# Kernel tuning notes

Measured on AMD Instinct MI355X. Metric: run time of the kernel, lower is better.

Reference implementation:

```python
import jax, jax.numpy as jnp
import numpy as np

NUM_HEADS = 16
HEAD_DIM = 64
LN_EPS = 1e-12


def _interleave_pairs(a, b):
    # stack([a, b], -1).reshape(..., 2*d) -> interleaved on last dim
    return jnp.stack([a, b], axis=-1).reshape(a.shape[:-1] + (a.shape[-1] * 2,))


def _rotate_half(x):
    # stack([-x[..., 1::2], x[..., ::2]], -1).reshape_as(x)
    return _interleave_pairs(-x[..., 1::2], x[..., ::2])


def setup_inputs() -> dict:
    key = jax.random.key(0)
    ks = jax.random.split(key, 4)
    B, S, H = 4, 2048, 1024
    hidden_states = jax.random.normal(ks[0], (B, S, H), dtype=jnp.float32)
    sinusoidal_pos = jax.random.uniform(ks[1], (1, 1, S, HEAD_DIM), dtype=jnp.float32)
    ln_weight = jnp.ones((H,), dtype=jnp.float32)
    ln_bias = jnp.zeros((H,), dtype=jnp.float32)
    w_qkv = jax.random.normal(ks[2], (H, 3 * H), dtype=jnp.float32) * (1.0 / np.sqrt(H))
    b_qkv = jax.random.normal(ks[3], (3 * H,), dtype=jnp.float32) * 0.02
    return {"hidden_states": hidden_states, "sinusoidal_pos": sinusoidal_pos,
            "ln_weight": ln_weight, "ln_bias": ln_bias, "w_qkv": w_qkv, "b_qkv": b_qkv}


def reference(hidden_states, sinusoidal_pos, ln_weight, ln_bias, w_qkv, b_qkv):
    B, S, H = hidden_states.shape
    # LayerNorm
    mu = jnp.mean(hidden_states, axis=-1, keepdims=True)
    var = jnp.mean(jnp.square(hidden_states - mu), axis=-1, keepdims=True)
    h = (hidden_states - mu) * jax.lax.rsqrt(var + LN_EPS) * ln_weight + ln_bias
    # Fused QKV projection
    qkv = h @ w_qkv + b_qkv                       # [B, S, 3H]
    q, k, v = jnp.split(qkv, 3, axis=-1)
    def to_heads(x):
        return x.reshape(B, S, NUM_HEADS, HEAD_DIM).transpose(0, 2, 1, 3)  # [B, Hn, S, D]
    q, k, v = to_heads(q), to_heads(k), to_heads(v)
    # RoPE (RoFormer interleaved style)
    sin, cos = jnp.split(sinusoidal_pos, 2, axis=-1)      # each [1,1,S,D/2]
    sin_pos = _interleave_pairs(sin, sin)                 # [1,1,S,D]
    cos_pos = _interleave_pairs(cos, cos)
    q = q * cos_pos + _rotate_half(q) * sin_pos
    k = k * cos_pos + _rotate_half(k) * sin_pos
    # SDPA (non-causal, no mask, eval-mode dropout=0)
    scale = 1.0 / np.sqrt(HEAD_DIM)
    scores = jnp.einsum('bhqd,bhkd->bhqk', q, k) * scale
    probs = jax.nn.softmax(scores, axis=-1)
    ctx = jnp.einsum('bhqk,bhkd->bhqd', probs, v)         # [B, Hn, S, D]
    ctx = ctx.transpose(0, 2, 1, 3).reshape(B, S, H)
    return ctx
```

## Files before the change

### kernel.cpp

```cpp
#include <hip/hip_runtime.h>
#include <hip/hip_bf16.h>
#include <cstdint>
#include <cstddef>

#define DEVINL __device__ __forceinline__

typedef float f32x2 __attribute__((ext_vector_type(2)));
typedef float f32x4 __attribute__((ext_vector_type(4)));
typedef float f32x16 __attribute__((ext_vector_type(16)));
typedef short s16x8 __attribute__((ext_vector_type(8)));
typedef short s16x4 __attribute__((ext_vector_type(4)));

static constexpr int Sd = 2048;
static constexpr int Hd = 1024;
static constexpr int NHd = 16;
static constexpr int Dd = 64;
static constexpr int N3 = 3072;

DEVINL float bf2f(short u){
  unsigned int t = ((unsigned int)(unsigned short)u) << 16;
  float f; __builtin_memcpy(&f, &t, 4); return f;
}
DEVINL short f2bf(float f){
  unsigned int t; __builtin_memcpy(&t, &f, 4);
  unsigned int r = t + 0x7FFFu + ((t >> 16) & 1u);
  return (short)(r >> 16);
}

DEVINL void gld16(const short* g, short* l){
  __builtin_amdgcn_global_load_lds((const __attribute__((address_space(1))) unsigned int*)g,
                                   (__attribute__((address_space(3))) unsigned int*)l, 16, 0, 0);
}

DEVINL int cvtpk(float lo, float hi){
  int r; asm("v_cvt_pk_bf16_f32 %0, %1, %2" : "=v"(r) : "v"(lo), "v"(hi)); return r;
}

DEVINL float fexp2(float x){
#if __has_builtin(__builtin_amdgcn_exp2f)
  return __builtin_amdgcn_exp2f(x);
#else
  return exp2f(x);
#endif
}

DEVINL f32x16 z16(){
  f32x16 v;
  #pragma unroll
  for (int i=0;i<16;i++) v[i]=0.f;
  return v;
}

__global__ __launch_bounds__(256) void ln_kernel(const float* __restrict__ x,
                                                 const float* __restrict__ w,
                                                 const float* __restrict__ bs,
                                                 short* __restrict__ h){
  int row = blockIdx.x, tid = threadIdx.x;
  const float* xr = x + (size_t)row * Hd;
  f32x4 v = *(const f32x4*)(xr + tid*4);
  float s1 = v[0]+v[1]+v[2]+v[3];
  float s2 = v[0]*v[0]+v[1]*v[1]+v[2]*v[2]+v[3]*v[3];
  #pragma unroll
  for (int off = 1; off < 64; off <<= 1){ s1 += __shfl_xor(s1, off); s2 += __shfl_xor(s2, off); }
  __shared__ float red[8];
  if ((tid & 63) == 0){ red[(tid>>6)*2] = s1; red[(tid>>6)*2+1] = s2; }
  __syncthreads();
  s1 = red[0]+red[2]+red[4]+red[6];
  s2 = red[1]+red[3]+red[5]+red[7];
  float mu = s1 * (1.0f/Hd);
  float rstd = rsqrtf(s2*(1.0f/Hd) - mu*mu + 1e-12f);
  f32x4 wv = *(const f32x4*)(w + tid*4);
  f32x4 bv = *(const f32x4*)(bs + tid*4);
  s16x4 o;
  #pragma unroll
  for (int i=0;i<4;i++) o[i] = f2bf((v[i]-mu)*rstd*wv[i] + bv[i]);
  *(s16x4*)(h + (size_t)row*Hd + tid*4) = o;
}

__global__ __launch_bounds__(256) void castw_kernel(const float* __restrict__ w, short* __restrict__ wT){
  __shared__ float t[32][33];
  int n0 = blockIdx.x*32, k0 = blockIdx.y*32;
  int tx = threadIdx.x, ty = threadIdx.y;
  #pragma unroll
  for (int i=0;i<4;i++) t[ty + i*8][tx] = w[(size_t)(k0 + ty + i*8)*N3 + n0 + tx];
  __syncthreads();
  #pragma unroll
  for (int i=0;i<4;i++) wT[(size_t)(n0 + ty + i*8)*Hd + k0 + tx] = f2bf(t[tx][ty + i*8]);
}

__global__ __launch_bounds__(256) void gemm_kernel(const short* __restrict__ A,
                                                   const short* __restrict__ Bt,
                                                   const float* __restrict__ bias,
                                                   const float* __restrict__ sp,
                                                   short* __restrict__ qo,
                                                   short* __restrict__ ko,
                                                   short* __restrict__ vo){
  __shared__ alignas(16) char smem[33792];
  short* lA = (short*)smem;
  short* lB = (short*)(smem + 8192);
  float* sps2 = (float*)smem;
  int bid = blockIdx.x;
  int xcd = bid & 7, idx = bid >> 3;
  int mt = xcd*8 + (idx & 7), nt = idx >> 3;
  int m0 = mt*128, n0 = nt*128;
  int tid = threadIdx.x, lane = tid & 63, wv = tid >> 6;
  int l15 = lane & 15, lq = lane >> 4;
  int wr = wv >> 1, wc = wv & 1;
  f32x4 zero = {0.f,0.f,0.f,0.f};
  f32x4 acc[4][4];
  #pragma unroll
  for (int m=0;m<4;m++)
    #pragma unroll
    for (int n=0;n<4;n++) acc[m][n] = zero;
  int flat = tid*8;
  int row0 = flat >> 5, col0 = flat & 31;
  const short* ga = A  + (size_t)(m0 + row0)*Hd + col0;
  const short* gb = Bt + (size_t)(n0 + row0)*Hd + col0;
  short* lAw = lA + wv*512;
  short* lBw = lB + wv*512;
  for (int kk = 0; kk < Hd; kk += 32){
    __syncthreads();
    gld16(ga + kk,                 lAw);
    gld16(ga + kk + (size_t)64*Hd, lAw + 2048);
    gld16(gb + kk,                 lBw);
    gld16(gb + kk + (size_t)64*Hd, lBw + 2048);
    __syncthreads();
    s16x8 af[4], bf[4];
    #pragma unroll
    for (int m=0;m<4;m++) af[m] = *(const s16x8*)(lA + (wr*64 + m*16 + l15)*32 + 8*lq);
    #pragma unroll
    for (int n=0;n<4;n++) bf[n] = *(const s16x8*)(lB + (wc*64 + n*16 + l15)*32 + 8*lq);
    #pragma unroll
    for (int m=0;m<4;m++)
      #pragma unroll
      for (int n=0;n<4;n++)
        acc[m][n] = __builtin_amdgcn_mfma_f32_16x16x32_bf16(af[m], bf[n], acc[m][n], 0, 0, 0);
  }
  int part = nt >> 3;
  if (part == 2){
    #pragma unroll
    for (int n=0;n<4;n++){
      int c = n0 + wc*64 + n*16 + l15;
      float bv = bias[c];
      int hh = (c >> 6) & 15, d = c & 63;
      #pragma unroll
      for (int m=0;m<4;m++){
        int r0 = m0 + wr*64 + m*16 + lq*4;
        int b = r0 >> 11, s0r = r0 & 2047;
        s16x4 o;
        #pragma unroll
        for (int j=0;j<4;j++) o[j] = f2bf(acc[m][n][j] + bv);
        *(s16x4*)(vo + (((size_t)((b*NHd + hh)*Dd + d)) << 11) + s0r) = o;
      }
    }
  } else {
    __syncthreads();
    const float* gsp = sp + (size_t)(m0 & 2047)*64;
    #pragma unroll
    for (int u4=0; u4<4; ++u4){
      int u = tid + u4*256;
      int sl = u >> 3, dh4 = u & 7;
      f32x4 s4v = *(const f32x4*)(gsp + sl*64 + dh4*4);
      f32x4 c4v = *(const f32x4*)(gsp + sl*64 + 32 + dh4*4);
      float* w8 = sps2 + sl*66 + dh4*8;
      f32x2 p0 = {s4v[0], c4v[0]}, p1 = {s4v[1], c4v[1]};
      f32x2 p2 = {s4v[2], c4v[2]}, p3 = {s4v[3], c4v[3]};
      *(f32x2*)(w8)     = p0; *(f32x2*)(w8 + 2) = p1;
      *(f32x2*)(w8 + 4) = p2; *(f32x2*)(w8 + 6) = p3;
    }
    __syncthreads();
    short* dst = part == 0 ? qo : ko;
    float postscale = part == 0 ? 0.18033688011112042f : 1.0f;
    float sgnmul = (l15 & 1) ? 1.0f : -1.0f;
    float bvv[4]; int hhv[4], dv[4];
    #pragma unroll
    for (int n=0;n<4;n++){
      int c = n0 + wc*64 + n*16 + l15;
      bvv[n] = bias[c]; hhv[n] = (c >> 6) & 15; dv[n] = c & 63;
    }
    int dh0 = l15 >> 1;
    #pragma unroll
    for (int m=0;m<4;m++){
      #pragma unroll
      for (int j=0;j<4;j++){
        int sl = wr*64 + m*16 + lq*4 + j;
        const float* sb = sps2 + sl*66 + dh0*2;
        int r = m0 + sl;
        int b = r >> 11, s = r & 2047;
        #pragma unroll
        for (int n=0;n<4;n++){
          f32x2 sc = *(const f32x2*)(sb + n*16);
          float x = acc[m][n][j] + bvv[n];
          float xp = __shfl_xor(x, 1);
          float y = (x*sc[1] + sgnmul*xp*sc[0]) * postscale;
          dst[(((size_t)((b*NHd + hhv[n])*Sd + s)) << 6) + dv[n]] = f2bf(y);
        }
      }
    }
  }
}

__global__ __launch_bounds__(512, 4) void attn_kernel(const short* __restrict__ q,
                                                      const short* __restrict__ k,
                                                      const short* __restrict__ vT,
                                                      float* __restrict__ out){
  __shared__ alignas(16) short kbuf[2][8192];
  __shared__ alignas(16) short vbuf[2][8192];
  int bid = blockIdx.x;
  int xcd = bid & 7, w = bid >> 3;
  int bh = xcd*8 + (w >> 3), qb = w & 7;
  int tid = threadIdx.x, lane = tid & 63, wv = tid >> 6;
  int l31 = lane & 31, hi = lane >> 5;
  const short* kp = k  + ((size_t)bh << 17);
  const short* vp = vT + ((size_t)bh << 17);
  int qrow = qb*256 + wv*32 + l31;
  const short* qp = q + ((size_t)bh << 17) + (size_t)qrow*64;
  s16x8 qf[4];
  #pragma unroll
  for (int kk=0;kk<4;kk++) qf[kk] = *(const s16x8*)(qp + kk*16 + hi*8);
  int kc0 = tid,      kr0 = kc0 >> 3;
  int kc1 = tid+512,  kr1 = kc1 >> 3;
  int koff0 = kr0*64 + ((kc0 ^ kr0) & 7)*8;
  int koff1 = kr1*64 + ((kc1 ^ kr1) & 7)*8;
  int vr0 = tid >> 4,       vcc0 = tid & 15;
  int vr1 = (tid+512) >> 4, vcc1 = (tid+512) & 15;
  int voff0 = vr0*2048 + ((vcc0 & 8) | ((vcc0 ^ vr0) & 7))*8;
  int voff1 = vr1*2048 + ((vcc1 & 8) | ((vcc1 ^ vr1) & 7))*8;

  f32x16 ot0 = z16(), ot1 = z16();
  float m = -1e30f, lr = 0.f;
  int rsw = (l31 & 7);

#define STAGE(nb, t) do { \
    gld16(kp + (size_t)(t)*8192 + koff0, &kbuf[nb][0]    + wv*512); \
    gld16(kp + (size_t)(t)*8192 + koff1, &kbuf[nb][4096] + wv*512); \
    gld16(vp + (size_t)(t)*128  + voff0, &vbuf[nb][0]    + wv*512); \
    gld16(vp + (size_t)(t)*128  + voff1, &vbuf[nb][4096] + wv*512); \
  } while(0)

  STAGE(0, 0);
  __syncthreads();

  for (int t = 0; t < 16; ++t){
    int cur = t & 1;
    if (t < 15) STAGE(cur^1, t+1);
    #pragma unroll
    for (int h = 0; h < 2; ++h){
      const short* kb = &kbuf[cur][h*4096];
      const short* vb = &vbuf[cur][h*64];
      f32x16 s0 = z16(), s1 = z16();
      __builtin_amdgcn_s_setprio(1);
      #pragma unroll
      for (int kk=0;kk<4;kk++){
        s16x8 kf0 = *(const s16x8*)(kb + l31*64       + (((kk*2 + hi) ^ rsw)*8));
        s0 = __builtin_amdgcn_mfma_f32_32x32x16_bf16(kf0, qf[kk], s0, 0, 0, 0);
        s16x8 kf1 = *(const s16x8*)(kb + (32+l31)*64  + (((kk*2 + hi) ^ rsw)*8));
        s1 = __builtin_amdgcn_mfma_f32_32x32x16_bf16(kf1, qf[kk], s1, 0, 0, 0);
      }
      __builtin_amdgcn_s_setprio(0);
      float tm[16];
      #pragma unroll
      for (int i=0;i<16;i++) tm[i] = fmaxf(s0[i], s1[i]);
      #pragma unroll
      for (int off=8; off>=1; off>>=1)
        #pragma unroll
        for (int i=0;i<off;i++) tm[i] = fmaxf(tm[i], tm[i+off]);
      float pmax = fmaxf(tm[0], __shfl_xor(tm[0], 32));
      if (!__all(pmax - m <= 8.0f)){
        float mn = fmaxf(m, pmax);
        float al = fexp2(m - mn);
        m = mn; lr *= al;
        #pragma unroll
        for (int i=0;i<16;i++){ ot0[i] *= al; ot1[i] *= al; }
      }
      #pragma unroll
      for (int i=0;i<16;i++){ s0[i] = fexp2(s0[i]-m); s1[i] = fexp2(s1[i]-m); }
      float ra[16];
      #pragma unroll
      for (int i=0;i<16;i++) ra[i] = s0[i] + s1[i];
      #pragma unroll
      for (int off=8; off>=1; off>>=1)
        #pragma unroll
        for (int i=0;i<off;i++) ra[i] += ra[i+off];
      lr += ra[0] + __shfl_xor(ra[0], 32);
      #pragma unroll
      for (int s4=0;s4<4;s4++){
        int base = (s4 & 1) * 8;
        int pkA0, pkA1, pkB0, pkB1;
        if (s4 < 2){
          pkA0 = cvtpk(s0[base],   s0[base+1]); pkA1 = cvtpk(s0[base+2], s0[base+3]);
          pkB0 = cvtpk(s0[base+4], s0[base+5]); pkB1 = cvtpk(s0[base+6], s0[base+7]);
        } else {
          pkA0 = cvtpk(s1[base],   s1[base+1]); pkA1 = cvtpk(s1[base+2], s1[base+3]);
          pkB0 = cvtpk(s1[base+4], s1[base+5]); pkB1 = cvtpk(s1[base+6], s1[base+7]);
        }
        int r0 = __shfl_xor(hi ? pkA0 : pkB0, 32);
        int r1 = __shfl_xor(hi ? pkA1 : pkB1, 32);
        union { int wq[4]; s16x8 v8; } u;
        u.wq[0] = hi ? r0   : pkA0;
        u.wq[1] = hi ? r1   : pkA1;
        u.wq[2] = hi ? pkB0 : r0;
        u.wq[3] = hi ? pkB1 : r1;
        __builtin_amdgcn_s_setprio(1);
        s16x8 vf0 = *(const s16x8*)(vb + l31*128      + (((s4*2 + hi) ^ rsw)*8));
        ot0 = __builtin_amdgcn_mfma_f32_32x32x16_bf16(vf0, u.v8, ot0, 0, 0, 0);
        s16x8 vf1 = *(const s16x8*)(vb + (32+l31)*128 + (((s4*2 + hi) ^ rsw)*8));
        ot1 = __builtin_amdgcn_mfma_f32_32x32x16_bf16(vf1, u.v8, ot1, 0, 0, 0);
        __builtin_amdgcn_s_setprio(0);
      }
    }
    __syncthreads();
  }
#undef STAGE
  float inv = 1.0f / lr;
  int b = bh >> 4, hh = bh & 15;
  float* orow = out + ((size_t)(b*Sd + qrow) << 10) + hh*64;
  #pragma unroll
  for (int g=0; g<4; ++g){
    f32x4 w0, w1;
    #pragma unroll
    for (int j=0;j<4;j++){ w0[j] = ot0[4*g+j]*inv; w1[j] = ot1[4*g+j]*inv; }
    *(f32x4*)(orow + g*8 + 4*hi)      = w0;
    *(f32x4*)(orow + 32 + g*8 + 4*hi) = w1;
  }
}

extern "C" void kernel_launch(void* const* d_in, const int* in_sizes, int n_in,
                              void* d_out, int out_size, void* d_ws, size_t ws_size,
                              hipStream_t stream){
  const float* hs = (const float*)d_in[0];
  const float* sp = (const float*)d_in[1];
  const float* lw = (const float*)d_in[2];
  const float* lb = (const float*)d_in[3];
  const float* wq = (const float*)d_in[4];
  const float* bq = (const float*)d_in[5];
  float* out = (float*)d_out;
  char* ws = (char*)d_ws;
  short* h   = (short*)(ws);
  short* wT  = (short*)(ws + 16777216);
  short* qb_ = (short*)(ws + 23068672);
  short* kb_ = (short*)(ws + 23068672 + 16777216);
  short* vTb = (short*)(ws + 23068672 + 33554432);

  hipLaunchKernelGGL(ln_kernel,    dim3(8192),    dim3(256),   0, stream, hs, lw, lb, h);
  hipLaunchKernelGGL(castw_kernel, dim3(96,32),   dim3(32,8),  0, stream, wq, wT);
  hipLaunchKernelGGL(gemm_kernel,  dim3(1536),    dim3(256),   0, stream, h, wT, bq, sp, qb_, kb_, vTb);
  hipLaunchKernelGGL(attn_kernel,  dim3(512),     dim3(512),   0, stream, qb_, kb_, vTb, out);
}
```

Baseline: 186.3 us.

## Process two 32-row query subtiles per wave in attention to reuse K/V fragments

```diff
diff --git a/kernel.cpp b/kernel.cpp
--- a/kernel.cpp
+++ b/kernel.cpp
@@ -200,7 +200,7 @@
   }
 }
 
-__global__ __launch_bounds__(512, 4) void attn_kernel(const short* __restrict__ q,
+__global__ __launch_bounds__(256, 2) void attn_kernel(const short* __restrict__ q,
                                                       const short* __restrict__ k,
                                                       const short* __restrict__ vT,
                                                       float* __restrict__ out){
@@ -213,29 +213,35 @@
   int l31 = lane & 31, hi = lane >> 5;
   const short* kp = k  + ((size_t)bh << 17);
   const short* vp = vT + ((size_t)bh << 17);
-  int qrow = qb*256 + wv*32 + l31;
-  const short* qp = q + ((size_t)bh << 17) + (size_t)qrow*64;
-  s16x8 qf[4];
-  #pragma unroll
-  for (int kk=0;kk<4;kk++) qf[kk] = *(const s16x8*)(qp + kk*16 + hi*8);
-  int kc0 = tid,      kr0 = kc0 >> 3;
-  int kc1 = tid+512,  kr1 = kc1 >> 3;
-  int koff0 = kr0*64 + ((kc0 ^ kr0) & 7)*8;
-  int koff1 = kr1*64 + ((kc1 ^ kr1) & 7)*8;
-  int vr0 = tid >> 4,       vcc0 = tid & 15;
-  int vr1 = (tid+512) >> 4, vcc1 = (tid+512) & 15;
-  int voff0 = vr0*2048 + ((vcc0 & 8) | ((vcc0 ^ vr0) & 7))*8;
-  int voff1 = vr1*2048 + ((vcc1 & 8) | ((vcc1 ^ vr1) & 7))*8;
-
-  f32x16 ot0 = z16(), ot1 = z16();
-  float m = -1e30f, lr = 0.f;
+  int qrowA = qb*256 + wv*64 + l31;
+  const short* qpA = q + ((size_t)bh << 17) + (size_t)qrowA*64;
+  s16x8 qf[2][4];
+  #pragma unroll
+  for (int kk=0;kk<4;kk++){
+    qf[0][kk] = *(const s16x8*)(qpA + kk*16 + hi*8);
+    qf[1][kk] = *(const s16x8*)(qpA + 2048 + kk*16 + hi*8);
+  }
+  int koff[4], voff[4];
+  #pragma unroll
+  for (int p=0;p<4;p++){
+    int c = p*256 + tid;
+    koff[p] = (c >> 3)*64 + ((c ^ (c >> 3)) & 7)*8;
+    int vr = c >> 4, vc = c & 15;
+    voff[p] = vr*2048 + ((vc & 8) | ((vc ^ vr) & 7))*8;
+  }
+
+  f32x16 ot0[2], ot1[2];
+  #pragma unroll
+  for (int qs=0;qs<2;qs++){ ot0[qs] = z16(); ot1[qs] = z16(); }
+  float m[2] = {-1e30f, -1e30f}, lr[2] = {0.f, 0.f};
   int rsw = (l31 & 7);
 
 #define STAGE(nb, t) do { \
-    gld16(kp + (size_t)(t)*8192 + koff0, &kbuf[nb][0]    + wv*512); \
-    gld16(kp + (size_t)(t)*8192 + koff1, &kbuf[nb][4096] + wv*512); \
-    gld16(vp + (size_t)(t)*128  + voff0, &vbuf[nb][0]    + wv*512); \
-    gld16(vp + (size_t)(t)*128  + voff1, &vbuf[nb][4096] + wv*512); \
+    _Pragma("unroll") \
+    for (int p=0;p<4;p++){ \
+      gld16(kp + (size_t)(t)*8192 + koff[p], &kbuf[nb][p*2048] + wv*512); \
+      gld16(vp + (size_t)(t)*128  + voff[p], &vbuf[nb][p*2048] + wv*512); \
+    } \
   } while(0)
 
   STAGE(0, 0);
@@ -248,80 +254,93 @@
     for (int h = 0; h < 2; ++h){
       const short* kb = &kbuf[cur][h*4096];
       const short* vb = &vbuf[cur][h*64];
-      f32x16 s0 = z16(), s1 = z16();
+      f32x16 s0[2], s1[2];
+      #pragma unroll
+      for (int qs=0;qs<2;qs++){ s0[qs] = z16(); s1[qs] = z16(); }
       __builtin_amdgcn_s_setprio(1);
       #pragma unroll
       for (int kk=0;kk<4;kk++){
         s16x8 kf0 = *(const s16x8*)(kb + l31*64       + (((kk*2 + hi) ^ rsw)*8));
-        s0 = __builtin_amdgcn_mfma_f32_32x32x16_bf16(kf0, qf[kk], s0, 0, 0, 0);
         s16x8 kf1 = *(const s16x8*)(kb + (32+l31)*64  + (((kk*2 + hi) ^ rsw)*8));
-        s1 = __builtin_amdgcn_mfma_f32_32x32x16_bf16(kf1, qf[kk], s1, 0, 0, 0);
+        s0[0] = __builtin_amdgcn_mfma_f32_32x32x16_bf16(kf0, qf[0][kk], s0[0], 0, 0, 0);
+        s1[0] = __builtin_amdgcn_mfma_f32_32x32x16_bf16(kf1, qf[0][kk], s1[0], 0, 0, 0);
+        s0[1] = __builtin_amdgcn_mfma_f32_32x32x16_bf16(kf0, qf[1][kk], s0[1], 0, 0, 0);
+        s1[1] = __builtin_amdgcn_mfma_f32_32x32x16_bf16(kf1, qf[1][kk], s1[1], 0, 0, 0);
       }
       __builtin_amdgcn_s_setprio(0);
-      float tm[16];
-      #pragma unroll
-      for (int i=0;i<16;i++) tm[i] = fmaxf(s0[i], s1[i]);
-      #pragma unroll
-      for (int off=8; off>=1; off>>=1)
-        #pragma unroll
-        for (int i=0;i<off;i++) tm[i] = fmaxf(tm[i], tm[i+off]);
-      float pmax = fmaxf(tm[0], __shfl_xor(tm[0], 32));
-      if (!__all(pmax - m <= 8.0f)){
-        float mn = fmaxf(m, pmax);
-        float al = fexp2(m - mn);
-        m = mn; lr *= al;
-        #pragma unroll
-        for (int i=0;i<16;i++){ ot0[i] *= al; ot1[i] *= al; }
-      }
-      #pragma unroll
-      for (int i=0;i<16;i++){ s0[i] = fexp2(s0[i]-m); s1[i] = fexp2(s1[i]-m); }
-      float ra[16];
-      #pragma unroll
-      for (int i=0;i<16;i++) ra[i] = s0[i] + s1[i];
-      #pragma unroll
-      for (int off=8; off>=1; off>>=1)
-        #pragma unroll
-        for (int i=0;i<off;i++) ra[i] += ra[i+off];
-      lr += ra[0] + __shfl_xor(ra[0], 32);
+      #pragma unroll
+      for (int qs=0;qs<2;qs++){
+        float tm[16];
+        #pragma unroll
+        for (int i=0;i<16;i++) tm[i] = fmaxf(s0[qs][i], s1[qs][i]);
+        #pragma unroll
+        for (int off=8; off>=1; off>>=1)
+          #pragma unroll
+          for (int i=0;i<off;i++) tm[i] = fmaxf(tm[i], tm[i+off]);
+        float pmax = fmaxf(tm[0], __shfl_xor(tm[0], 32));
+        if (!__all(pmax - m[qs] <= 8.0f)){
+          float mn = fmaxf(m[qs], pmax);
+          float al = fexp2(m[qs] - mn);
+          m[qs] = mn; lr[qs] *= al;
+          #pragma unroll
+          for (int i=0;i<16;i++){ ot0[qs][i] *= al; ot1[qs][i] *= al; }
+        }
+        #pragma unroll
+        for (int i=0;i<16;i++){ s0[qs][i] = fexp2(s0[qs][i]-m[qs]); s1[qs][i] = fexp2(s1[qs][i]-m[qs]); }
+        float ra[16];
+        #pragma unroll
+        for (int i=0;i<16;i++) ra[i] = s0[qs][i] + s1[qs][i];
+        #pragma unroll
+        for (int off=8; off>=1; off>>=1)
+          #pragma unroll
+          for (int i=0;i<off;i++) ra[i] += ra[i+off];
+        lr[qs] += ra[0] + __shfl_xor(ra[0], 32);
+      }
       #pragma unroll
       for (int s4=0;s4<4;s4++){
+        s16x8 vf0 = *(const s16x8*)(vb + l31*128      + (((s4*2 + hi) ^ rsw)*8));
+        s16x8 vf1 = *(const s16x8*)(vb + (32+l31)*128 + (((s4*2 + hi) ^ rsw)*8));
         int base = (s4 & 1) * 8;
-        int pkA0, pkA1, pkB0, pkB1;
-        if (s4 < 2){
-          pkA0 = cvtpk(s0[base],   s0[base+1]); pkA1 = cvtpk(s0[base+2], s0[base+3]);
-          pkB0 = cvtpk(s0[base+4], s0[base+5]); pkB1 = cvtpk(s0[base+6], s0[base+7]);
-        } else {
-          pkA0 = cvtpk(s1[base],   s1[base+1]); pkA1 = cvtpk(s1[base+2], s1[base+3]);
-          pkB0 = cvtpk(s1[base+4], s1[base+5]); pkB1 = cvtpk(s1[base+6], s1[base+7]);
+        #pragma unroll
+        for (int qs=0;qs<2;qs++){
+          int pkA0, pkA1, pkB0, pkB1;
+          if (s4 < 2){
+            pkA0 = cvtpk(s0[qs][base],   s0[qs][base+1]); pkA1 = cvtpk(s0[qs][base+2], s0[qs][base+3]);
+            pkB0 = cvtpk(s0[qs][base+4], s0[qs][base+5]); pkB1 = cvtpk(s0[qs][base+6], s0[qs][base+7]);
+          } else {
+            pkA0 = cvtpk(s1[qs][base],   s1[qs][base+1]); pkA1 = cvtpk(s1[qs][base+2], s1[qs][base+3]);
+            pkB0 = cvtpk(s1[qs][base+4], s1[qs][base+5]); pkB1 = cvtpk(s1[qs][base+6], s1[qs][base+7]);
+          }
+          int r0 = __shfl_xor(hi ? pkA0 : pkB0, 32);
+          int r1 = __shfl_xor(hi ? pkA1 : pkB1, 32);
+          union { int wq[4]; s16x8 v8; } u;
+          u.wq[0] = hi ? r0   : pkA0;
+          u.wq[1] = hi ? r1   : pkA1;
+          u.wq[2] = hi ? pkB0 : r0;
+          u.wq[3] = hi ? pkB1 : r1;
+          __builtin_amdgcn_s_setprio(1);
+          ot0[qs] = __builtin_amdgcn_mfma_f32_32x32x16_bf16(vf0, u.v8, ot0[qs], 0, 0, 0);
+          ot1[qs] = __builtin_amdgcn_mfma_f32_32x32x16_bf16(vf1, u.v8, ot1[qs], 0, 0, 0);
+          __builtin_amdgcn_s_setprio(0);
         }
-        int r0 = __shfl_xor(hi ? pkA0 : pkB0, 32);
-        int r1 = __shfl_xor(hi ? pkA1 : pkB1, 32);
-        union { int wq[4]; s16x8 v8; } u;
-        u.wq[0] = hi ? r0   : pkA0;
-        u.wq[1] = hi ? r1   : pkA1;
-        u.wq[2] = hi ? pkB0 : r0;
-        u.wq[3] = hi ? pkB1 : r1;
-        __builtin_amdgcn_s_setprio(1);
-        s16x8 vf0 = *(const s16x8*)(vb + l31*128      + (((s4*2 + hi) ^ rsw)*8));
-        ot0 = __builtin_amdgcn_mfma_f32_32x32x16_bf16(vf0, u.v8, ot0, 0, 0, 0);
-        s16x8 vf1 = *(const s16x8*)(vb + (32+l31)*128 + (((s4*2 + hi) ^ rsw)*8));
-        ot1 = __builtin_amdgcn_mfma_f32_32x32x16_bf16(vf1, u.v8, ot1, 0, 0, 0);
-        __builtin_amdgcn_s_setprio(0);
       }
     }
     __syncthreads();
   }
 #undef STAGE
-  float inv = 1.0f / lr;
   int b = bh >> 4, hh = bh & 15;
-  float* orow = out + ((size_t)(b*Sd + qrow) << 10) + hh*64;
-  #pragma unroll
-  for (int g=0; g<4; ++g){
-    f32x4 w0, w1;
-    #pragma unroll
-    for (int j=0;j<4;j++){ w0[j] = ot0[4*g+j]*inv; w1[j] = ot1[4*g+j]*inv; }
-    *(f32x4*)(orow + g*8 + 4*hi)      = w0;
-    *(f32x4*)(orow + 32 + g*8 + 4*hi) = w1;
+  #pragma unroll
+  for (int qs=0;qs<2;qs++){
+    float inv = 1.0f / lr[qs];
+    float* orow = out + ((size_t)(b*Sd + qrowA + qs*32) << 10) + hh*64;
+    #pragma unroll
+    for (int g=0; g<4; ++g){
+      f32x4 w0, w1;
+      #pragma unroll
+      for (int j=0;j<4;j++){ w0[j] = ot0[qs][4*g+j]*inv; w1[j] = ot1[qs][4*g+j]*inv; }
+      *(f32x4*)(orow + g*8 + 4*hi)      = w0;
+      *(f32x4*)(orow + 32 + g*8 + 4*hi) = w1;
+    }
   }
 }
 
@@ -345,5 +364,5 @@
   hipLaunchKernelGGL(ln_kernel,    dim3(8192),    dim3(256),   0, stream, hs, lw, lb, h);
   hipLaunchKernelGGL(castw_kernel, dim3(96,32),   dim3(32,8),  0, stream, wq, wT);
   hipLaunchKernelGGL(gemm_kernel,  dim3(1536),    dim3(256),   0, stream, h, wT, bq, sp, qb_, kb_, vTb);
-  hipLaunchKernelGGL(attn_kernel,  dim3(512),     dim3(512),   0, stream, qb_, kb_, vTb, out);
-}
+  hipLaunchKernelGGL(attn_kernel,  dim3(512),     dim3(256),   0, stream, qb_, kb_, vTb, out);
+}
```

Result: slower. 190.2 us (+2.1%).

## Triple-buffer QKV GEMM LDS tiles with async prefetch and XOR swizzle

Applied to the files above, without the earlier changes.

```diff
diff --git a/kernel.cpp b/kernel.cpp
--- a/kernel.cpp
+++ b/kernel.cpp
@@ -95,9 +95,7 @@
                                                    short* __restrict__ qo,
                                                    short* __restrict__ ko,
                                                    short* __restrict__ vo){
-  __shared__ alignas(16) char smem[33792];
-  short* lA = (short*)smem;
-  short* lB = (short*)(smem + 8192);
+  __shared__ alignas(16) char smem[49152];
   float* sps2 = (float*)smem;
   int bid = blockIdx.x;
   int xcd = bid & 7, idx = bid >> 3;
@@ -112,30 +110,63 @@
   for (int m=0;m<4;m++)
     #pragma unroll
     for (int n=0;n<4;n++) acc[m][n] = zero;
-  int flat = tid*8;
-  int row0 = flat >> 5, col0 = flat & 31;
-  const short* ga = A  + (size_t)(m0 + row0)*Hd + col0;
-  const short* gb = Bt + (size_t)(n0 + row0)*Hd + col0;
-  short* lAw = lA + wv*512;
-  short* lBw = lB + wv*512;
-  for (int kk = 0; kk < Hd; kk += 32){
-    __syncthreads();
-    gld16(ga + kk,                 lAw);
-    gld16(ga + kk + (size_t)64*Hd, lAw + 2048);
-    gld16(gb + kk,                 lBw);
-    gld16(gb + kk + (size_t)64*Hd, lBw + 2048);
-    __syncthreads();
-    s16x8 af[4], bf[4];
-    #pragma unroll
-    for (int m=0;m<4;m++) af[m] = *(const s16x8*)(lA + (wr*64 + m*16 + l15)*32 + 8*lq);
-    #pragma unroll
-    for (int n=0;n<4;n++) bf[n] = *(const s16x8*)(lB + (wc*64 + n*16 + l15)*32 + 8*lq);
-    #pragma unroll
-    for (int m=0;m<4;m++)
-      #pragma unroll
-      for (int n=0;n<4;n++)
-        acc[m][n] = __builtin_amdgcn_mfma_f32_16x16x32_bf16(af[m], bf[n], acc[m][n], 0, 0, 0);
+  int rA = tid >> 2;
+  int gA = (tid & 3) ^ ((rA >> 1) & 3);
+  const short* gaA0 = A  + (size_t)(m0 + rA)*Hd + gA*8;
+  const short* gaA1 = gaA0 + (size_t)64*Hd;
+  const short* gaB0 = Bt + (size_t)(n0 + rA)*Hd + gA*8;
+  const short* gaB1 = gaB0 + (size_t)64*Hd;
+  int rsw2 = (l15 >> 1) & 3;
+  int fcol = (lq ^ rsw2) * 8;
+  int arow = (wr*64 + l15)*32 + fcol;
+  int brow = (wc*64 + l15)*32 + fcol;
+
+#define GSTAGE(bq_, t_) do { \
+    short* dA = (short*)(smem + (bq_)*16384) + wv*512; \
+    short* dB = (short*)(smem + (bq_)*16384 + 8192) + wv*512; \
+    gld16(gaA0 + (t_)*32, dA); \
+    gld16(gaA1 + (t_)*32, dA + 2048); \
+    gld16(gaB0 + (t_)*32, dB); \
+    gld16(gaB1 + (t_)*32, dB + 2048); \
+  } while(0)
+
+#define KBODY(bq_) do { \
+    const short* Ab = (const short*)(smem + (bq_)*16384); \
+    const short* Bb = (const short*)(smem + (bq_)*16384 + 8192); \
+    s16x8 af[4], bf[4]; \
+    _Pragma("unroll") \
+    for (int m=0;m<4;m++) af[m] = *(const s16x8*)(Ab + arow + m*512); \
+    _Pragma("unroll") \
+    for (int n=0;n<4;n++) bf[n] = *(const s16x8*)(Bb + brow + n*512); \
+    __builtin_amdgcn_s_setprio(1); \
+    _Pragma("unroll") \
+    for (int m=0;m<4;m++) \
+      _Pragma("unroll") \
+      for (int n=0;n<4;n++) \
+        acc[m][n] = __builtin_amdgcn_mfma_f32_16x16x32_bf16(af[m], bf[n], acc[m][n], 0, 0, 0); \
+    __builtin_amdgcn_s_setprio(0); \
+  } while(0)
+
+  GSTAGE(0, 0);
+  GSTAGE(1, 1);
+  int bq = 0;
+  for (int t = 0; t < 31; ++t){
+    asm volatile("s_waitcnt vmcnt(4)" ::: "memory");
+    __builtin_amdgcn_s_barrier();
+    __builtin_amdgcn_sched_barrier(0);
+    if (t < 30){
+      int bn = bq + 2; if (bn >= 3) bn -= 3;
+      GSTAGE(bn, t+2);
+    }
+    KBODY(bq);
+    ++bq; if (bq >= 3) bq = 0;
   }
+  asm volatile("s_waitcnt vmcnt(0)" ::: "memory");
+  __builtin_amdgcn_s_barrier();
+  __builtin_amdgcn_sched_barrier(0);
+  KBODY(bq);
+#undef GSTAGE
+#undef KBODY
   int part = nt >> 3;
   if (part == 2){
     #pragma unroll
```

Measured after the change: 176.3 us. 1.06x faster.
